# Kernel optimization log

Measured on AMD Instinct MI355X. Metric: run time of the kernel, lower is better.

Reference implementation:

```python
import jax, jax.numpy as jnp
import numpy as np

RADIUS = 5.0          # cutoff radius (Angstrom)
MAX_NBR = 32          # max_num_neighbors_threshold
CELL_L = 12.0         # cubic box edge; > 2*RADIUS/2 so rep=1 (27 image cells)


def setup_inputs() -> dict:
    key = jax.random.key(0)
    k1, _ = jax.random.split(key)
    B, N = 16, 256
    pos = jax.random.uniform(k1, (B, N, 3), dtype=jnp.float32) * CELL_L
    cell = jnp.tile(jnp.eye(3, dtype=jnp.float32)[None] * CELL_L, (B, 1, 1))
    return {"pos": pos, "cell": cell}


def reference(pos, cell):
    # pos: [B,N,3] atom positions, cell: [B,3,3] lattice vectors (rows a1,a2,a3)
    B, N, _ = pos.shape
    # periodic image offsets n in {-1,0,1}^3 -> unit: [C,3], C=27
    r = jnp.arange(-1, 2, dtype=pos.dtype)
    n1, n2, n3 = jnp.meshgrid(r, r, r, indexing="ij")
    unit = jnp.stack([n1.ravel(), n2.ravel(), n3.ravel()], axis=-1)  # [C,3]
    C = unit.shape[0]
    # pbc_offsets[b,c,:] = sum_k n_k * a_k  (== bmm(cell^T, unit^T) in torch code)
    offsets = jnp.einsum("ck,bkd->bcd", unit, cell)  # [B,C,3]
    # candidate edge vectors: receiver i, source j shifted by image offset c
    dvec = pos[:, :, None, None, :] - (pos[:, None, :, None, :] + offsets[:, None, None, :, :])  # [B,N,N,C,3]
    dsqr = jnp.sum(dvec * dvec, axis=-1)  # [B,N,N,C]
    # radius mask + remove self (atom_distance_sqr > 1e-4)
    within = (dsqr <= RADIUS * RADIUS) & (dsqr > 1e-4)
    M = N * C
    dsqr_f = jnp.where(within, dsqr, jnp.inf).reshape(B, N, M)
    # per-receiver sort-based top-K truncation (mirrors get_max_neighbors_mask:
    # index_copy into [num_atoms, max_nbr] padded with inf, sort, keep first K finite)
    order = jnp.argsort(dsqr_f, axis=-1)
    rank = jnp.argsort(order, axis=-1)           # rank of each candidate among its receiver's neighbors
    keep = (rank < MAX_NBR) & jnp.isfinite(dsqr_f)  # [B,N,M] final edge mask
    dist = jnp.where(keep, jnp.sqrt(jnp.where(keep, dsqr_f, 1.0)), 0.0)  # masked edge lengths
    dvec_m = jnp.where(keep[..., None], dvec.reshape(B, N, M, 3), 0.0)   # masked edge vectors
    # num_neighbors_image == segment_csr(clamp(num_neighbors, K)) == per-image kept-edge count
    num_neighbors_image = jnp.sum(keep.reshape(B, -1), axis=-1).astype(jnp.int32)
    return dist, dvec_m, num_neighbors_image
```

## Files before the change

kernel.cpp:

```cpp
#include <hip/hip_runtime.h>
#include <stdint.h>


constexpr int B_ = 16, N_ = 256, C_ = 27;
constexpr int M_ = N_ * C_;
constexpr int MAXC = 256;
constexpr int KMAX = 32;

__global__ __launch_bounds__(256)
void nbr_kernel(const float* __restrict__ pos,
                const float* __restrict__ cell,
                float* __restrict__ dist,
                float* __restrict__ dvec,
                float* __restrict__ nn)
{
#pragma clang fp contract(off)
    __shared__ float offx[C_], offy[C_], offz[C_];
    __shared__ unsigned long long keys[MAXC];
    __shared__ float4 vals[MAXC];
    __shared__ int cnt;

    const int bi  = blockIdx.x;
    const int b   = bi >> 8;
    const int i   = bi & 255;
    const int tid = threadIdx.x;

    const float* pb = pos + b * N_ * 3;
    const float pjx = pb[tid * 3 + 0], pjy = pb[tid * 3 + 1], pjz = pb[tid * 3 + 2];
    const float pix = pb[i * 3 + 0], piy = pb[i * 3 + 1], piz = pb[i * 3 + 2];

    if (tid < C_) {
        const float n1 = (float)(tid / 9 - 1);
        const float n2 = (float)((tid / 3) % 3 - 1);
        const float n3 = (float)(tid % 3 - 1);
        const float* cb = cell + b * 9;
        offx[tid] = n1 * cb[0] + n2 * cb[3] + n3 * cb[6];
        offy[tid] = n1 * cb[1] + n2 * cb[4] + n3 * cb[7];
        offz[tid] = n1 * cb[2] + n2 * cb[5] + n3 * cb[8];
    }
    if (tid == 0) cnt = 0;
    __syncthreads();

    float* __restrict__ drow = dist + (size_t)bi * M_;
    float* __restrict__ vrow = dvec + (size_t)bi * (size_t)(M_ * 3);

    {
        const float4 z = make_float4(0.f, 0.f, 0.f, 0.f);
        float4* dp = (float4*)drow;
        float4* vp = (float4*)vrow;
        for (int t = tid; t < M_ / 4; t += 256) dp[t] = z;
        for (int t = tid; t < 3 * M_ / 4; t += 256) vp[t] = z;
    }

    #pragma unroll 1
    for (int c = 0; c < C_; ++c) {
        const float sx = pjx + offx[c], sy = pjy + offy[c], sz = pjz + offz[c];
        const float dx = pix - sx, dy = piy - sy, dz = piz - sz;
        const float dsq = dx * dx + dy * dy + dz * dz;
        if (dsq <= 25.0f && dsq > 1e-4f) {
            const int idx = atomicAdd(&cnt, 1);
            if (idx < MAXC) {
                keys[idx] = ((unsigned long long)__float_as_uint(dsq) << 32)
                          | (unsigned)(tid * C_ + c);
                vals[idx] = make_float4(dx, dy, dz, dsq);
            }
        }
    }
    __syncthreads();

    int K = cnt; if (K > MAXC) K = MAXC;
    if (tid == 0)
        atomicAdd(&nn[b], (float)(K < KMAX ? K : KMAX));

    for (int idx = tid; idx < K; idx += 256) {
        const unsigned long long key = keys[idx];
        int r = 0;
        for (int q = 0; q < K; ++q) r += (keys[q] < key) ? 1 : 0;
        if (r < KMAX) {
            const int m = (int)(key & 0xffffffffu);
            const float4 v = vals[idx];
            drow[m]         = sqrtf(v.w);
            vrow[m * 3 + 0] = v.x;
            vrow[m * 3 + 1] = v.y;
            vrow[m * 3 + 2] = v.z;
        }
    }
}

extern "C" void kernel_launch(void* const* d_in, const int* in_sizes, int n_in,
                              void* d_out, int out_size, void* d_ws, size_t ws_size,
                              hipStream_t stream)
{
    const float* pos  = (const float*)d_in[0];
    const float* cell = (const float*)d_in[1];
    float* dist = (float*)d_out;
    float* dvec = dist + (size_t)B_ * N_ * M_;
    float* nn   = dvec + (size_t)B_ * N_ * M_ * 3;
    hipMemsetAsync(nn, 0, B_ * sizeof(float), stream);
    nbr_kernel<<<dim3(B_ * N_), dim3(256), 0, stream>>>(pos, cell, dist, dvec, nn);
}
```

Measured before the change: 472.3 us.

## Zero outputs with bulk memset and scatter kept edges in a separate kernel

Per-block float4 zeroing of the dist and dvec rows is replaced by one hipMemsetAsync over the whole output buffer. The neighbor kernel now appends kept edges (flat index and values) to a compact workspace list through a global atomic counter. A second kernel then scatters those entries into the zeroed outputs. The aim is to move the large zero-fill onto the memset engine and take stores out of the compute kernel, at the cost of two extra launches, a global atomic and a workspace round trip.

```diff
diff --git a/kernel.cpp b/kernel.cpp
--- a/kernel.cpp
+++ b/kernel.cpp
@@ -6,13 +6,15 @@
 constexpr int M_ = N_ * C_;
 constexpr int MAXC = 256;
 constexpr int KMAX = 32;
+constexpr int EMAX = B_ * N_ * KMAX;
 
 __global__ __launch_bounds__(256)
-void nbr_kernel(const float* __restrict__ pos,
-                const float* __restrict__ cell,
-                float* __restrict__ dist,
-                float* __restrict__ dvec,
-                float* __restrict__ nn)
+void edges_kernel(const float* __restrict__ pos,
+                  const float* __restrict__ cell,
+                  float* __restrict__ nn,
+                  int*   __restrict__ ectr,
+                  int*   __restrict__ eidx,
+                  float4* __restrict__ evals)
 {
 #pragma clang fp contract(off)
     __shared__ float offx[C_], offy[C_], offz[C_];
@@ -27,7 +29,7 @@
 
     const float* pb = pos + b * N_ * 3;
     const float pjx = pb[tid * 3 + 0], pjy = pb[tid * 3 + 1], pjz = pb[tid * 3 + 2];
-    const float pix = pb[i * 3 + 0], piy = pb[i * 3 + 1], piz = pb[i * 3 + 2];
+    const float pix = pb[i * 3 + 0],   piy = pb[i * 3 + 1],   piz = pb[i * 3 + 2];
 
     if (tid < C_) {
         const float n1 = (float)(tid / 9 - 1);
@@ -40,17 +42,6 @@
     }
     if (tid == 0) cnt = 0;
     __syncthreads();
-
-    float* __restrict__ drow = dist + (size_t)bi * M_;
-    float* __restrict__ vrow = dvec + (size_t)bi * (size_t)(M_ * 3);
-
-    {
-        const float4 z = make_float4(0.f, 0.f, 0.f, 0.f);
-        float4* dp = (float4*)drow;
-        float4* vp = (float4*)vrow;
-        for (int t = tid; t < M_ / 4; t += 256) dp[t] = z;
-        for (int t = tid; t < 3 * M_ / 4; t += 256) vp[t] = z;
-    }
 
     #pragma unroll 1
     for (int c = 0; c < C_; ++c) {
@@ -77,14 +68,28 @@
         int r = 0;
         for (int q = 0; q < K; ++q) r += (keys[q] < key) ? 1 : 0;
         if (r < KMAX) {
-            const int m = (int)(key & 0xffffffffu);
-            const float4 v = vals[idx];
-            drow[m]         = sqrtf(v.w);
-            vrow[m * 3 + 0] = v.x;
-            vrow[m * 3 + 1] = v.y;
-            vrow[m * 3 + 2] = v.z;
+            const int e = atomicAdd(ectr, 1);
+            eidx[e]  = bi * M_ + (int)(key & 0xffffffffu);
+            evals[e] = vals[idx];
         }
     }
+}
+
+__global__ __launch_bounds__(256)
+void scatter_kernel(const int* __restrict__ ectr,
+                    const int* __restrict__ eidx,
+                    const float4* __restrict__ evals,
+                    float* __restrict__ dist,
+                    float* __restrict__ dvec)
+{
+    const int e = blockIdx.x * 256 + threadIdx.x;
+    if (e >= *ectr) return;
+    const int id = eidx[e];
+    const float4 v = evals[e];
+    dist[id] = sqrtf(v.w);
+    dvec[3 * (size_t)id + 0] = v.x;
+    dvec[3 * (size_t)id + 1] = v.y;
+    dvec[3 * (size_t)id + 2] = v.z;
 }
 
 extern "C" void kernel_launch(void* const* d_in, const int* in_sizes, int n_in,
@@ -96,6 +101,13 @@
     float* dist = (float*)d_out;
     float* dvec = dist + (size_t)B_ * N_ * M_;
     float* nn   = dvec + (size_t)B_ * N_ * M_ * 3;
-    hipMemsetAsync(nn, 0, B_ * sizeof(float), stream);
-    nbr_kernel<<<dim3(B_ * N_), dim3(256), 0, stream>>>(pos, cell, dist, dvec, nn);
+
+    int*    ectr  = (int*)d_ws;
+    int*    eidx  = (int*)((char*)d_ws + 128);
+    float4* evals = (float4*)((char*)d_ws + 128 + (size_t)EMAX * 4);
+
+    hipMemsetAsync(d_out, 0, (size_t)out_size * sizeof(float), stream);
+    hipMemsetAsync(d_ws, 0, 128, stream);
+    edges_kernel<<<dim3(B_ * N_), dim3(256), 0, stream>>>(pos, cell, nn, ectr, eidx, evals);
+    scatter_kernel<<<dim3(EMAX / 256), dim3(256), 0, stream>>>(ectr, eidx, evals, dist, dvec);
 }
```

Result: slower. 562.4 us (+19.1%).
